# Kernel tuning notes

Hardware: AMD Instinct MI355X
Metric: run time of the kernel (lower is better)

## Reference

```python
import jax, jax.numpy as jnp
import numpy as np

T, B, X, F, Z, H = 64, 512, 784, 64, 64, 512


def _lin(v, W, b):
    return v @ W.T + b


def _gru(xt, h, Wih, Whh, bih, bhh):
    # PyTorch GRUCell gate math
    gi = xt @ Wih.T + bih
    gh = h @ Whh.T + bhh
    ir, iz, in_ = jnp.split(gi, 3, axis=-1)
    hr, hz, hn = jnp.split(gh, 3, axis=-1)
    r = jax.nn.sigmoid(ir + hr)
    z = jax.nn.sigmoid(iz + hz)
    n = jnp.tanh(in_ + r * hn)
    return (1.0 - z) * n + z * h


def _kld(mu1, sd1, mu2, sd2):
    r = sd1 / sd2
    return 0.5 * jnp.sum(((mu1 - mu2) / sd2) ** 2 + r ** 2 - 2.0 * jnp.log(r) - 1.0)


def setup_inputs() -> dict:
    key = jax.random.key(0)
    ks = iter(jax.random.split(key, 64))

    def Wn(*shape):
        return 0.02 * jax.random.normal(next(ks), shape, jnp.float32)

    d = {}
    d["x"] = jax.random.uniform(next(ks), (T, B, X), jnp.float32)
    d["eps_f"] = jax.random.normal(next(ks), (B, F), jnp.float32)
    d["eps_z"] = jax.random.normal(next(ks), (T, B, Z), jnp.float32)
    d.update(
        pxW1=Wn(H, X), pxb1=Wn(H), pxW2=Wn(H, H), pxb2=Wn(H),
        pzW=Wn(H, Z), pzb=Wn(H),
        pfW=Wn(H, F), pfb=Wn(H),
        rWih=Wn(3 * H, 3 * H), rWhh=Wn(3 * H, H), rbih=Wn(3 * H), rbhh=Wn(3 * H),
        zpW=Wn(H, H), zpb=Wn(H), zpmW=Wn(Z, H), zpmb=Wn(Z), zpsW=Wn(Z, H), zpsb=Wn(Z),
        feWih=Wn(3 * H, H), feWhh=Wn(3 * H, H), febih=Wn(3 * H), febhh=Wn(3 * H),
        femW=Wn(F, H), femb=Wn(F), fesW=Wn(F, H), fesb=Wn(F),
        zeW1=Wn(H, 2 * H), zeb1=Wn(H), zeW2=Wn(H, H), zeb2=Wn(H),
        zemW=Wn(Z, H), zemb=Wn(Z), zesW=Wn(Z, H), zesb=Wn(Z),
        dW1=Wn(H, 3 * H), db1=Wn(H), dW2=Wn(H, H), db2=Wn(H),
        dmW=Wn(X, H), dmb=Wn(X),
    )
    return d


def reference(x, eps_f, eps_z, pxW1, pxb1, pxW2, pxb2, pzW, pzb, pfW, pfb,
              rWih, rWhh, rbih, rbhh, zpW, zpb, zpmW, zpmb, zpsW, zpsb,
              feWih, feWhh, febih, febhh, femW, femb, fesW, fesb,
              zeW1, zeb1, zeW2, zeb2, zemW, zemb, zesW, zesb,
              dW1, db1, dW2, db2, dmW, dmb):
    relu = jax.nn.relu
    # phi_x over all timesteps at once: [T, B, H]
    phi_x = relu(_lin(relu(_lin(x, pxW1, pxb1)), pxW2, pxb2))
    h0 = jnp.zeros((x.shape[1], H), x.dtype)

    # f encoder GRU over the sequence; only the final hidden is used
    f_h, _ = jax.lax.scan(
        lambda h, xt: (_gru(xt, h, feWih, feWhh, febih, febhh), None), h0, phi_x)
    f_mean = _lin(f_h, femW, femb)
    f_std = jax.nn.softplus(_lin(f_h, fesW, fesb))
    f = eps_f * f_std + f_mean
    phi_f = relu(_lin(f, pfW, pfb))
    f_kld = _kld(f_mean, f_std, jnp.zeros_like(f_mean), jnp.ones_like(f_std))

    def step(carry, inp):
        h, zk, nll = carry
        px_t, e_t, x_t = inp
        zp = relu(_lin(h, zpW, zpb))
        zpm = _lin(zp, zpmW, zpmb)
        zps = jax.nn.softplus(_lin(zp, zpsW, zpsb))
        ze = relu(_lin(relu(_lin(jnp.concatenate([px_t, h], 1), zeW1, zeb1)), zeW2, zeb2))
        zem = _lin(ze, zemW, zemb)
        zes = jax.nn.softplus(_lin(ze, zesW, zesb))
        z_t = e_t * zes + zem
        phi_z = relu(_lin(z_t, pzW, pzb))
        dec = relu(_lin(relu(_lin(jnp.concatenate([phi_z, phi_f, h], 1), dW1, db1)), dW2, db2))
        dec_mean = jax.nn.sigmoid(_lin(dec, dmW, dmb))
        h_new = _gru(jnp.concatenate([px_t, phi_z, phi_f], 1), h, rWih, rWhh, rbih, rbhh)
        zk = zk + _kld(zem, zes, zpm, zps)
        nll = nll - jnp.sum(x_t * jnp.log(dec_mean) + (1.0 - x_t) * jnp.log(1.0 - dec_mean))
        return (h_new, zk, nll), None

    zero = jnp.zeros((), x.dtype)
    (_, z_kld, nll), _ = jax.lax.scan(step, (h0, zero, zero), (phi_x, eps_z, x))
    return (f_kld, z_kld, nll)
```

## Files before the change

kernel.cpp:

```cpp
#include <hip/hip_runtime.h>
#include <cmath>

namespace {

constexpr int Tn = 64;
constexpr int Bn = 512;
constexpr int Xn = 784;
constexpr int XnP = 800;
constexpr int Fn = 64;
constexpr int Zn = 64;
constexpr int Hn = 512;

typedef unsigned short us;
typedef __attribute__((ext_vector_type(8))) short bf16x8;
typedef __attribute__((ext_vector_type(4))) float f32x4;

__device__ __forceinline__ us f2b(float v) {
  unsigned int u = __float_as_uint(v);
  return (us)((u + 0x7FFFu + ((u >> 16) & 1u)) >> 16);
}
__device__ __forceinline__ float b2f(us u) { return __uint_as_float(((unsigned int)u) << 16); }
__device__ __forceinline__ float sigmf(float v) { return 1.0f / (1.0f + __expf(-v)); }
__device__ __forceinline__ float splusf(float v) {
  return v > 0.0f ? (v + log1pf(__expf(-v))) : log1pf(__expf(v));
}
__device__ __forceinline__ float block_sum(float v, float* red) {
  #pragma unroll
  for (int off = 32; off > 0; off >>= 1) v += __shfl_down(v, off, 64);
  if ((threadIdx.x & 63) == 0) red[threadIdx.x >> 6] = v;
  __syncthreads();
  float s = 0.0f;
  if (threadIdx.x == 0) s = red[0] + red[1] + red[2] + red[3];
  return s;
}

__global__ void cvt(const float* __restrict__ s, us* __restrict__ d, int n) {
  int i = blockIdx.x * 256 + threadIdx.x;
  if (i < n) d[i] = f2b(s[i]);
}
__global__ void cvt_pad(const float* __restrict__ s, us* __restrict__ d, int C, int Cp, int n) {
  int i = blockIdx.x * 256 + threadIdx.x;
  if (i < n) {
    int r = i / Cp, c = i - r * Cp;
    d[i] = (c < C) ? f2b(s[(size_t)r * C + c]) : (us)0;
  }
}

template <int NSEG, bool RELU, bool F32OUT, bool HASINIT, bool HASBIAS>
__device__ void tile_gemmx(
    int bx, int by,
    const us* A0, const us* W0, int ldw0, int K0,
    const us* A1, const us* W1, int ldw1, int K1,
    const float* initC, int ldi, const float* bias,
    void* Cout, int ldc, char* smemc)
{
  us* As = (us*)smemc; us* Bs = (us*)(smemc + 5120);
  const int tid = threadIdx.x, srow = tid >> 2, scb = (tid & 3) * 8;
  const int lane = tid & 63, w = tid >> 6, l15 = lane & 15, q = lane >> 4;
  const int m0 = by * 64, n0 = bx * 64;
  f32x4 acc[4];
  if (HASINIT) {
    #pragma unroll
    for (int j = 0; j < 4; ++j)
      #pragma unroll
      for (int r = 0; r < 4; ++r)
        acc[j][r] = initC[(size_t)(m0 + w * 16 + q * 4 + r) * ldi + n0 + j * 16 + l15];
  } else {
    #pragma unroll
    for (int j = 0; j < 4; ++j) acc[j] = (f32x4){0.f, 0.f, 0.f, 0.f};
  }
  #pragma unroll
  for (int seg = 0; seg < NSEG; ++seg) {
    const us* A = (seg == 0) ? A0 : A1;
    const us* W = (seg == 0) ? W0 : W1;
    const int ldw = (seg == 0) ? ldw0 : ldw1;
    const int K   = (seg == 0) ? K0 : K1;
    const us* ap = A + (size_t)(m0 + srow) * K + scb;
    const us* wp = W + (size_t)(n0 + srow) * ldw + scb;
    uint4 av = *(const uint4*)ap;
    uint4 wv = *(const uint4*)wp;
    for (int k0 = 0; k0 < K; k0 += 32) {
      __syncthreads();
      *(uint4*)&As[srow * 40 + scb] = av;
      *(uint4*)&Bs[srow * 40 + scb] = wv;
      __syncthreads();
      if (k0 + 32 < K) {
        av = *(const uint4*)(ap + k0 + 32);
        wv = *(const uint4*)(wp + k0 + 32);
      }
      bf16x8 a = *(const bf16x8*)&As[(w * 16 + l15) * 40 + q * 8];
      #pragma unroll
      for (int j = 0; j < 4; ++j) {
        bf16x8 b = *(const bf16x8*)&Bs[(j * 16 + l15) * 40 + q * 8];
        acc[j] = __builtin_amdgcn_mfma_f32_16x16x32_bf16(a, b, acc[j], 0, 0, 0);
      }
    }
  }
  #pragma unroll
  for (int j = 0; j < 4; ++j) {
    const int col = n0 + j * 16 + l15;
    const float bv = HASBIAS ? bias[col] : 0.f;
    #pragma unroll
    for (int r = 0; r < 4; ++r) {
      const int row = m0 + w * 16 + q * 4 + r;
      float v = acc[j][r] + bv;
      if (RELU) v = fmaxf(v, 0.f);
      if (F32OUT) ((float*)Cout)[(size_t)row * ldc + col] = v;
      else        ((us*)Cout)[(size_t)row * ldc + col] = f2b(v);
    }
  }
}

__device__ void tile_gru_fe(
    int bx, int by,
    const us* A0, const us* Wih,
    const us* hprev, const us* Whh,
    const float* bih, const float* bhh,
    us* hnew, char* smemc)
{
  us* Asm = (us*)smemc; us* Rs = (us*)(smemc + 5120);
  us* Zs = (us*)(smemc + 10240); us* Ns = (us*)(smemc + 15360);
  const int tid = threadIdx.x, srow = tid >> 2, scb = (tid & 3) * 8;
  const int lane = tid & 63, w = tid >> 6, l15 = lane & 15, q = lane >> 4;
  const int m0 = by * 64, c0 = bx * 64;
  f32x4 aR[4], aZ[4], aI[4], aH[4];
  #pragma unroll
  for (int j = 0; j < 4; ++j) {
    aR[j] = (f32x4){0.f, 0.f, 0.f, 0.f}; aZ[j] = aR[j]; aI[j] = aR[j]; aH[j] = aR[j];
  }
  #pragma unroll
  for (int seg = 0; seg < 2; ++seg) {
    const bool hseg = (seg == 1);
    const us* A  = hseg ? hprev : A0;
    const us* Wb = hseg ? Whh : Wih;
    const us* ap = A + (size_t)(m0 + srow) * Hn + scb;
    const us* wr = Wb + (size_t)(c0 + srow) * Hn + scb;
    const us* wz = wr + (size_t)Hn * Hn;
    const us* wn = wz + (size_t)Hn * Hn;
    uint4 av = *(const uint4*)ap;
    uint4 rv = *(const uint4*)wr;
    uint4 zv = *(const uint4*)wz;
// ... 24 lines not shown
      }
    }
  }
  #pragma unroll
  for (int j = 0; j < 4; ++j) {
    const int c = c0 + j * 16 + l15;
    const float bR = bih[c] + bhh[c];
    const float bZ = bih[Hn + c] + bhh[Hn + c];
    const float bI = bih[2 * Hn + c];
    const float bH = bhh[2 * Hn + c];
    #pragma unroll
    for (int r = 0; r < 4; ++r) {
      const int m = m0 + w * 16 + q * 4 + r;
      const float h = b2f(hprev[(size_t)m * Hn + c]);
      const float rg = sigmf(aR[j][r] + bR);
      const float zg = sigmf(aZ[j][r] + bZ);
      const float ng = tanhf(aI[j][r] + bI + rg * (aH[j][r] + bH));
      hnew[(size_t)m * Hn + c] = f2b((1.0f - zg) * ng + zg * h);
    }
  }
}

__device__ void tile_gru_fin(
    int bx, int by,
    const us* phiz, const us* rWih,
    const float* gipre, const float* ghpre,
    const us* hprev,
    const float* bih, const float* bhh,
    us* hnew, char* smemc)
{
  us* Asm = (us*)smemc; us* Rs = (us*)(smemc + 5120);
  us* Zs = (us*)(smemc + 10240); us* Ns = (us*)(smemc + 15360);
  const int tid = threadIdx.x, srow = tid >> 2, scb = (tid & 3) * 8;
  const int lane = tid & 63, w = tid >> 6, l15 = lane & 15, q = lane >> 4;
  const int m0 = by * 64, c0 = bx * 64;
  f32x4 aR[4], aZ[4], aI[4];
  float aH[4][4];
  #pragma unroll
  for (int j = 0; j < 4; ++j) {
    const int c = c0 + j * 16 + l15;
    #pragma unroll
    for (int r = 0; r < 4; ++r) {
      const size_t row = (size_t)(m0 + w * 16 + q * 4 + r) * 1536;
      aR[j][r] = gipre[row + c] + ghpre[row + c];
      aZ[j][r] = gipre[row + 512 + c] + ghpre[row + 512 + c];
      aI[j][r] = gipre[row + 1024 + c];
      aH[j][r] = ghpre[row + 1024 + c];
    }
  }
  const us* ap = phiz + (size_t)(m0 + srow) * Hn + scb;
  const us* wr = rWih + (size_t)(c0 + srow) * 1536 + 512 + scb;
  const us* wz = wr + (size_t)512 * 1536;
// ... 26 lines not shown
      aI[j] = __builtin_amdgcn_mfma_f32_16x16x32_bf16(a, bn, aI[j], 0, 0, 0);
    }
  }
  #pragma unroll
  for (int j = 0; j < 4; ++j) {
    const int c = c0 + j * 16 + l15;
    const float bR = bih[c] + bhh[c];
    const float bZ = bih[Hn + c] + bhh[Hn + c];
    const float bI = bih[2 * Hn + c];
    const float bH = bhh[2 * Hn + c];
    #pragma unroll
    for (int r = 0; r < 4; ++r) {
      const int m = m0 + w * 16 + q * 4 + r;
      const float h = b2f(hprev[(size_t)m * Hn + c]);
      const float rg = sigmf(aR[j][r] + bR);
      const float zg = sigmf(aZ[j][r] + bZ);
      const float ng = tanhf(aI[j][r] + bI + rg * (aH[j][r] + bH));
      hnew[(size_t)m * Hn + c] = f2b((1.0f - zg) * ng + zg * h);
    }
  }
}

__device__ void tile_nll(
    int bx, int by,
    const us* dec, const us* dmW, const float* dmb, const float* xt,
    float* nll, char* smemc)
{
  us* As = (us*)smemc; us* Bs = (us*)(smemc + 5120);
  float* red = (float*)(smemc + 10240);
  const int tid = threadIdx.x, srow = tid >> 2, scb = (tid & 3) * 8;
  const int lane = tid & 63, w = tid >> 6, l15 = lane & 15, q = lane >> 4;
  const int m0 = by * 64, n0 = bx * 64;
  f32x4 acc[4];
  #pragma unroll
  for (int j = 0; j < 4; ++j) acc[j] = (f32x4){0.f, 0.f, 0.f, 0.f};
  const int wrow = (n0 + srow < Xn) ? (n0 + srow) : (Xn - 1);
  const us* ap = dec + (size_t)(m0 + srow) * Hn + scb;
  const us* wp = dmW + (size_t)wrow * Hn + scb;
  uint4 av = *(const uint4*)ap;
  uint4 wv = *(const uint4*)wp;
  for (int k0 = 0; k0 < Hn; k0 += 32) {
    __syncthreads();
    *(uint4*)&As[srow * 40 + scb] = av;
    *(uint4*)&Bs[srow * 40 + scb] = wv;
    __syncthreads();
    if (k0 + 32 < Hn) {
      av = *(const uint4*)(ap + k0 + 32);
      wv = *(const uint4*)(wp + k0 + 32);
    }
// ... 6 lines not shown
  }
  float sum = 0.0f;
  #pragma unroll
  for (int j = 0; j < 4; ++j) {
    const int n = n0 + j * 16 + l15;
    if (n < Xn) {
      const float bv = dmb[n];
      #pragma unroll
      for (int r = 0; r < 4; ++r) {
        const int m = m0 + w * 16 + q * 4 + r;
        const float a = acc[j][r] + bv;
        const float xv = xt[(size_t)m * Xn + n];
        sum += splusf(-a) + (1.0f - xv) * a;
      }
    }
  }
  const float s = block_sum(sum, red);
  if (tid == 0) atomicAdd(nll, s);
}

template <int MODE>
__device__ void stat_dual(int vb,
    const us* Ain, const us* Wm, const float* bm, const us* Ws, const float* bs,
    const float* eps, const float* pm_in, const float* ps_in,
    us* o0b, float* o_pm, float* o_ps, float* kacc, char* smemc)
{
  us* As = (us*)smemc; us* Ms = (us*)(smemc + 5120); us* Ss = (us*)(smemc + 10240);
  float* red = (float*)(smemc + 15360);
  const int tid = threadIdx.x, srow = tid >> 2, scb = (tid & 3) * 8;
  const int lane = tid & 63, w = tid >> 6, l15 = lane & 15, q = lane >> 4;
  const int m0 = vb * 64;
  f32x4 am[4], as_[4];
  #pragma unroll
  for (int j = 0; j < 4; ++j) { am[j] = (f32x4){0.f, 0.f, 0.f, 0.f}; as_[j] = am[j]; }
  const us* ap = Ain + (size_t)(m0 + srow) * Hn + scb;
  const us* mp = Wm + (size_t)srow * Hn + scb;
  const us* sp = Ws + (size_t)srow * Hn + scb;
  uint4 av = *(const uint4*)ap;
  uint4 mv = *(const uint4*)mp;
  uint4 sv = *(const uint4*)sp;
  for (int k0 = 0; k0 < Hn; k0 += 32) {
    __syncthreads();
    *(uint4*)&As[srow * 40 + scb] = av;
    *(uint4*)&Ms[srow * 40 + scb] = mv;
    *(uint4*)&Ss[srow * 40 + scb] = sv;
    __syncthreads();
    if (k0 + 32 < Hn) {
      av = *(const uint4*)(ap + k0 + 32);
// ... 4 lines not shown
    #pragma unroll
    for (int j = 0; j < 4; ++j) {
      bf16x8 b0 = *(const bf16x8*)&Ms[(j * 16 + l15) * 40 + q * 8];
      bf16x8 b1 = *(const bf16x8*)&Ss[(j * 16 + l15) * 40 + q * 8];
      am[j]  = __builtin_amdgcn_mfma_f32_16x16x32_bf16(a, b0, am[j], 0, 0, 0);
      as_[j] = __builtin_amdgcn_mfma_f32_16x16x32_bf16(a, b1, as_[j], 0, 0, 0);
    }
  }
  float kld = 0.0f;
  #pragma unroll
  for (int j = 0; j < 4; ++j) {
    const int c = j * 16 + l15;
    const float bmv = bm[c], bsv = bs[c];
    #pragma unroll
    for (int r = 0; r < 4; ++r) {
      const int m = m0 + w * 16 + q * 4 + r;
      const float mu = am[j][r] + bmv;
      const float sd = splusf(as_[j][r] + bsv);
      if (MODE == 0) {
        o_pm[(size_t)m * Zn + c] = mu;
        o_ps[(size_t)m * Zn + c] = sd;
      } else {
        o0b[(size_t)m * Zn + c] = f2b(eps[(size_t)m * Zn + c] * sd + mu);
        if (MODE == 1) {
          kld += mu * mu + sd * sd - 2.0f * __logf(sd) - 1.0f;
        } else {
          const float pm = pm_in[(size_t)m * Zn + c];
          const float ps = ps_in[(size_t)m * Zn + c];
          const float dd = (mu - pm) / ps;
          const float rr = sd / ps;
          kld += dd * dd + rr * rr - 2.0f * __logf(rr) - 1.0f;
        }
      }
    }
  }
  if (MODE != 0) {
    const float s = block_sum(kld, red);
    if (tid == 0) atomicAdd(kacc, 0.5f * s);
  }
}

__global__ __launch_bounds__(256) void k_gemmA(
    const us* A, const us* W, int ldw, int K, const float* bias, us* C, int ldc)
{
  __shared__ alignas(16) char sm[10240];
  tile_gemmx<1, true, false, false, true>(blockIdx.x, blockIdx.y, A, W, ldw, K,
      nullptr, nullptr, 0, 0, nullptr, 0, bias, C, ldc, sm);
}

__global__ __launch_bounds__(256) void k_gruB(
    const us* A0, const us* Wih, const us* hprev, const us* Whh,
    const float* bih, const float* bhh, us* hnew)
{
  __shared__ alignas(16) char sm[20480];
  tile_gru_fe(blockIdx.x, blockIdx.y, A0, Wih, hprev, Whh, bih, bhh, hnew, sm);
}

__global__ __launch_bounds__(256) void k_statf(
    const us* fh, const us* femW, const float* femb, const us* fesW, const float* fesb,
    const float* eps_f, us* fbuf, float* kacc)
{
  __shared__ alignas(16) char sm[15376];
  stat_dual<1>(blockIdx.x, fh, femW, femb, fesW, fesb, eps_f,
               nullptr, nullptr, fbuf, nullptr, nullptr, kacc, sm);
}

__global__ __launch_bounds__(256) void kP2(
    const us* phi_f, const us* rWih, const us* dW1, const float* db1,
    float* Cpre_gru, float* Cpre_dec)
{
  __shared__ alignas(16) char sm[10240];
  const int b = blockIdx.x;
  if (b < 192)
    tile_gemmx<1, false, true, false, false>(b % 24, b / 24, phi_f, rWih + 1024, 1536, Hn,
        nullptr, nullptr, 0, 0, nullptr, 0, nullptr, Cpre_gru, 1536, sm);
  else
    tile_gemmx<1, false, true, false, true>((b - 192) & 7, (b - 192) >> 3,
        phi_f, dW1 + 512, 1536, Hn,
        nullptr, nullptr, 0, 0, nullptr, 0, db1, Cpre_dec, 512, sm);
}

__global__ __launch_bounds__(256) void kP3(
    const us* h0, const us* zpW, const float* zpb, us* zp,
    const us* px0, const us* zeW1, const float* zeb1, us* zepre)
{
  __shared__ alignas(16) char sm[10240];
  const int b = blockIdx.x;
  if (b < 64)
    tile_gemmx<1, true, false, false, true>(b & 7, b >> 3, h0, zpW, Hn, Hn,
        nullptr, nullptr, 0, 0, nullptr, 0, zpb, zp, Hn, sm);
  else
    tile_gemmx<2, true, false, false, true>((b - 64) & 7, (b - 64) >> 3,
        px0, zeW1, 1024, Hn, h0, zeW1 + 512, 1024, Hn,
        nullptr, 0, zeb1, zepre, Hn, sm);
}

__global__ __launch_bounds__(256) void kP4(
    const us* zepre, const us* zeW2, const float* zeb2, us* ze,
    const us* zp, const us* zpmW, const float* zpmb, const us* zpsW, const float* zpsb,
    float* zpm, float* zps)
{
  __shared__ alignas(16) char sm[15376];
  const int b = blockIdx.x;
  if (b < 64)
    tile_gemmx<1, true, false, false, true>(b & 7, b >> 3, zepre, zeW2, Hn, Hn,
        nullptr, nullptr, 0, 0, nullptr, 0, zeb2, ze, Hn, sm);
  else
    stat_dual<0>(b - 64, zp, zpmW, zpmb, zpsW, zpsb,
                 nullptr, nullptr, nullptr, nullptr, zpm, zps, nullptr, sm);
}

__global__ __launch_bounds__(256) void kS1(
    const us* ze, const us* zemW, const float* zemb, const us* zesW, const float* zesb,
    const float* eps_zt, const float* zpm, const float* zps, us* zt, float* kacc,
    const us* px_t, const us* rWih, const float* Cpre_gru, float* gipre)
{
  __shared__ alignas(16) char sm[15376];
  const int b = blockIdx.x;
  if (b < 8)
    stat_dual<2>(b, ze, zemW, zemb, zesW, zesb, eps_zt, zpm, zps,
                 zt, nullptr, nullptr, kacc, sm);
  else {
    const int tb = b - 8;
    tile_gemmx<1, false, true, true, false>(tb % 24, tb / 24, px_t, rWih, 1536, Hn,
        nullptr, nullptr, 0, 0, Cpre_gru, 1536, nullptr, gipre, 1536, sm);
  }
}

__global__ __launch_bounds__(256) void kS2(
    const us* zt, const us* pzW, const float* pzb, us* phiz)
{
  __shared__ alignas(16) char sm[10240];
  tile_gemmx<1, true, false, false, true>(blockIdx.x & 7, blockIdx.x >> 3, zt, pzW, Zn, Zn,
      nullptr, nullptr, 0, 0, nullptr, 0, pzb, phiz, Hn, sm);
}

__global__ __launch_bounds__(256) void kS3(
    const us* phiz, const us* rWih, const float* gipre, const float* ghpre,
    const us* hprev, const float* rbih, const float* rbhh, us* hnew,
    const us* dW1, const float* dtmph, us* dtmp)
{
  __shared__ alignas(16) char sm[20480];
  const int b = blockIdx.x;
  if (b < 64)
    tile_gru_fin(b & 7, b >> 3, phiz, rWih, gipre, ghpre, hprev, rbih, rbhh, hnew, sm);
  else
    tile_gemmx<1, true, false, true, false>((b - 64) & 7, (b - 64) >> 3, phiz, dW1, 1536, Hn,
        nullptr, nullptr, 0, 0, dtmph, 512, nullptr, dtmp, Hn, sm);
}

__global__ __launch_bounds__(256) void kS4(
    const us* dtmp, const us* dW2, const float* db2, us* dec,
    const us* hnext, const us* zpW, const float* zpb, us* zp,
    const us* px1, const us* zeW1, const float* zeb1, us* zepre,
    const us* dW1, const float* Cpre_dec, float* dtmph)
{
  __shared__ alignas(16) char sm[10240];
  const int b = blockIdx.x;
  if (b < 64)
    tile_gemmx<1, true, false, false, true>(b & 7, b >> 3, dtmp, dW2, Hn, Hn,
        nullptr, nullptr, 0, 0, nullptr, 0, db2, dec, Hn, sm);
  else if (b < 128)
    tile_gemmx<1, true, false, false, true>((b - 64) & 7, (b - 64) >> 3, hnext, zpW, Hn, Hn,
        nullptr, nullptr, 0, 0, nullptr, 0, zpb, zp, Hn, sm);
  else if (b < 192)
    tile_gemmx<2, true, false, false, true>((b - 128) & 7, (b - 128) >> 3,
        px1, zeW1, 1024, Hn, hnext, zeW1 + 512, 1024, Hn,
        nullptr, 0, zeb1, zepre, Hn, sm);
  else
    tile_gemmx<1, false, true, true, false>((b - 192) & 7, (b - 192) >> 3,
        hnext, dW1 + 1024, 1536, Hn,
        nullptr, nullptr, 0, 0, Cpre_dec, 512, nullptr, dtmph, 512, sm);
}

__global__ __launch_bounds__(256) void kS5(
    const us* dec, const us* dmW, const float* dmb, const float* xt, float* nll,
    const us* zepre, const us* zeW2, const float* zeb2, us* ze,
    const us* zp, const us* zpmW, const float* zpmb, const us* zpsW, const float* zpsb,
    float* zpm, float* zps,
    const us* hnext, const us* rWhh, float* ghpre)
{
  __shared__ alignas(16) char sm[15376];
  const int b = blockIdx.x;
  if (b < 104)
    tile_nll(b % 13, b / 13, dec, dmW, dmb, xt, nll, sm);
  else if (b < 168)
    tile_gemmx<1, true, false, false, true>((b - 104) & 7, (b - 104) >> 3, zepre, zeW2, Hn, Hn,
        nullptr, nullptr, 0, 0, nullptr, 0, zeb2, ze, Hn, sm);
  else if (b < 176)
    stat_dual<0>(b - 168, zp, zpmW, zpmb, zpsW, zpsb,
                 nullptr, nullptr, nullptr, nullptr, zpm, zps, nullptr, sm);
  else {
    const int tb = b - 176;
    tile_gemmx<1, false, true, false, false>(tb % 24, tb / 24, hnext, rWhh, Hn, Hn,
        nullptr, nullptr, 0, 0, nullptr, 0, nullptr, ghpre, 1536, sm);
  }
}

}

extern "C" void kernel_launch(void* const* d_in, const int* in_sizes, int n_in,
                              void* d_out, int out_size, void* d_ws, size_t ws_size,
                              hipStream_t stream)
{
  (void)in_sizes; (void)n_in; (void)out_size;
  const float* x     = (const float*)d_in[0];
  const float* eps_f = (const float*)d_in[1];
  const float* eps_z = (const float*)d_in[2];
  const float* pxW1  = (const float*)d_in[3];
  const float* pxb1  = (const float*)d_in[4];
  const float* pxW2  = (const float*)d_in[5];
  const float* pxb2  = (const float*)d_in[6];
  const float* pzW   = (const float*)d_in[7];
  const float* pzb   = (const float*)d_in[8];
  const float* pfW   = (const float*)d_in[9];
  const float* pfb   = (const float*)d_in[10];
  const float* rWih  = (const float*)d_in[11];
  const float* rWhh  = (const float*)d_in[12];
  const float* rbih  = (const float*)d_in[13];
  const float* rbhh  = (const float*)d_in[14];
  const float* zpW   = (const float*)d_in[15];
  const float* zpb   = (const float*)d_in[16];
  const float* zpmW  = (const float*)d_in[17];
  const float* zpmb  = (const float*)d_in[18];
  const float* zpsW  = (const float*)d_in[19];
  const float* zpsb  = (const float*)d_in[20];
  const float* feWih = (const float*)d_in[21];
  const float* feWhh = (const float*)d_in[22];
// ... 28 lines not shown
  };

  us* b_pxW1  = (us*)ab((size_t)512 * XnP * 2);
  us* b_pxW2  = (us*)ab((size_t)512 * 512 * 2);
  us* b_pzW   = (us*)ab((size_t)512 * 64 * 2);
  us* b_pfW   = (us*)ab((size_t)512 * 64 * 2);
  us* b_rWih  = (us*)ab((size_t)1536 * 1536 * 2);
  us* b_rWhh  = (us*)ab((size_t)1536 * 512 * 2);
  us* b_zpW   = (us*)ab((size_t)512 * 512 * 2);
  us* b_zpmW  = (us*)ab((size_t)64 * 512 * 2);
  us* b_zpsW  = (us*)ab((size_t)64 * 512 * 2);
  us* b_feWih = (us*)ab((size_t)1536 * 512 * 2);
  us* b_feWhh = (us*)ab((size_t)1536 * 512 * 2);
  us* b_femW  = (us*)ab((size_t)64 * 512 * 2);
  us* b_fesW  = (us*)ab((size_t)64 * 512 * 2);
  us* b_zeW1  = (us*)ab((size_t)512 * 1024 * 2);
  us* b_zeW2  = (us*)ab((size_t)512 * 512 * 2);
  us* b_zemW  = (us*)ab((size_t)64 * 512 * 2);
  us* b_zesW  = (us*)ab((size_t)64 * 512 * 2);
  us* b_dW1   = (us*)ab((size_t)512 * 1536 * 2);
  us* b_dW2   = (us*)ab((size_t)512 * 512 * 2);
  us* b_dmW   = (us*)ab((size_t)Xn * 512 * 2);

  us* phi_x = (us*)ab((size_t)Tn * Bn * Hn * 2);
  us* fh_a  = (us*)ab((size_t)Bn * Hn * 2);
  us* h_a   = (us*)ab((size_t)Bn * Hn * 2);
  us* fh_b  = (us*)ab((size_t)Bn * Hn * 2);
  us* h_b   = (us*)ab((size_t)Bn * Hn * 2);
  us* fbuf  = (us*)ab((size_t)Bn * Fn * 2);
  us* phi_f = (us*)ab((size_t)Bn * Hn * 2);
  us* zp    = (us*)ab((size_t)Bn * Hn * 2);
  us* zepre = (us*)ab((size_t)Bn * Hn * 2);
  us* ze    = (us*)ab((size_t)Bn * Hn * 2);
  us* zt    = (us*)ab((size_t)Bn * Zn * 2);
  us* phiz  = (us*)ab((size_t)Bn * Hn * 2);
  us* dtmp  = (us*)ab((size_t)Bn * Hn * 2);
  us* dec   = (us*)ab((size_t)Bn * Hn * 2);
  float* zpm = (float*)ab((size_t)Bn * Zn * 4);
  float* zps = (float*)ab((size_t)Bn * Zn * 4);
  float* Cpre_gru = (float*)ab((size_t)Bn * 1536 * 4);
  float* Cpre_dec = (float*)ab((size_t)Bn * 512 * 4);
  float* gipre    = (float*)ab((size_t)Bn * 1536 * 4);
  float* ghpre    = (float*)ab((size_t)Bn * 1536 * 4);
  float* dtmph    = (float*)ab((size_t)Bn * 512 * 4);

  int CH = 16;
  while (CH > 1 && off + (size_t)CH * (Bn * XnP + Bn * Hn) * 2 + 4096 > ws_size) CH >>= 1;
  us* xch  = (us*)ab((size_t)CH * Bn * XnP * 2);
  us* tmpb = (us*)ab((size_t)CH * Bn * Hn * 2);

  hipMemsetAsync(d_out, 0, 3 * sizeof(float), stream);
  hipMemsetAsync(fh_a, 0, 2 * (size_t)Bn * Hn * 2, stream);
  hipMemsetAsync(ghpre, 0, (size_t)Bn * 1536 * 4, stream);

  const dim3 blk(256);
  auto CVT = [&](const float* s, us* d, size_t n) {
    cvt<<<dim3((unsigned)((n + 255) / 256)), blk, 0, stream>>>(s, d, (int)n);
  };

  {
    const size_t n = (size_t)512 * XnP;
    cvt_pad<<<dim3((unsigned)((n + 255) / 256)), blk, 0, stream>>>(pxW1, b_pxW1, Xn, XnP, (int)n);
  }
  CVT(pxW2, b_pxW2, (size_t)512 * 512);
  CVT(pzW, b_pzW, (size_t)512 * 64);
  CVT(pfW, b_pfW, (size_t)512 * 64);
  CVT(rWih, b_rWih, (size_t)1536 * 1536);
  CVT(rWhh, b_rWhh, (size_t)1536 * 512);
  CVT(zpW, b_zpW, (size_t)512 * 512);
  CVT(zpmW, b_zpmW, (size_t)64 * 512);
  CVT(zpsW, b_zpsW, (size_t)64 * 512);
  CVT(feWih, b_feWih, (size_t)1536 * 512);
  CVT(feWhh, b_feWhh, (size_t)1536 * 512);
  CVT(femW, b_femW, (size_t)64 * 512);
  CVT(fesW, b_fesW, (size_t)64 * 512);
  CVT(zeW1, b_zeW1, (size_t)512 * 1024);
  CVT(zeW2, b_zeW2, (size_t)512 * 512);
  CVT(zemW, b_zemW, (size_t)64 * 512);
  CVT(zesW, b_zesW, (size_t)64 * 512);
  CVT(dW1, b_dW1, (size_t)512 * 1536);
  CVT(dW2, b_dW2, (size_t)512 * 512);
  CVT(dmW, b_dmW, (size_t)Xn * 512);

  for (int c = 0; c < Tn / CH; ++c) {
    const size_t nx = (size_t)CH * Bn * XnP;
    cvt_pad<<<dim3((unsigned)((nx + 255) / 256)), blk, 0, stream>>>(
        x + (size_t)c * CH * Bn * Xn, xch, Xn, XnP, (int)nx);
    const dim3 gA(8, CH * Bn / 64);
    k_gemmA<<<gA, blk, 0, stream>>>(xch, b_pxW1, XnP, XnP, pxb1, tmpb, Hn);
    k_gemmA<<<gA, blk, 0, stream>>>(tmpb, b_pxW2, Hn, Hn, pxb2,
                                    phi_x + (size_t)c * CH * Bn * Hn, Hn);
  }

  us* fc = fh_a; us* fn2 = fh_b;
  for (int t = 0; t < Tn; ++t) {
    k_gruB<<<dim3(8, 8), blk, 0, stream>>>(
        phi_x + (size_t)t * Bn * Hn, b_feWih, fc, b_feWhh, febih, febhh, fn2);
    us* sw = fc; fc = fn2; fn2 = sw;
  }

  k_statf<<<dim3(8), blk, 0, stream>>>(fh_a, b_femW, femb, b_fesW, fesb, eps_f, fbuf, out + 0);

  k_gemmA<<<dim3(8, 8), blk, 0, stream>>>(fbuf, b_pfW, Fn, Fn, pfb, phi_f, Hn);
  kP2<<<dim3(256), blk, 0, stream>>>(phi_f, b_rWih, b_dW1, db1, Cpre_gru, Cpre_dec);
  hipMemcpyAsync(dtmph, Cpre_dec, (size_t)Bn * 512 * 4, hipMemcpyDeviceToDevice, stream);
  kP3<<<dim3(128), blk, 0, stream>>>(h_a, b_zpW, zpb, zp, phi_x, b_zeW1, zeb1, zepre);
  kP4<<<dim3(72), blk, 0, stream>>>(zepre, b_zeW2, zeb2, ze,
                                    zp, b_zpmW, zpmb, b_zpsW, zpsb, zpm, zps);

  for (int t = 0; t < Tn; ++t) {
    const us* hcur = (t & 1) ? h_b : h_a;
    us* hnext      = (t & 1) ? h_a : h_b;
    const bool last = (t == Tn - 1);
    const us* px_t = phi_x + (size_t)t * Bn * Hn;

    kS1<<<dim3(200), blk, 0, stream>>>(
        ze, b_zemW, zemb, b_zesW, zesb, eps_z + (size_t)t * Bn * Zn, zpm, zps,
        zt, out + 1, px_t, b_rWih, Cpre_gru, gipre);

    kS2<<<dim3(64), blk, 0, stream>>>(zt, b_pzW, pzb, phiz);

    kS3<<<dim3(128), blk, 0, stream>>>(
        phiz, b_rWih, gipre, ghpre, hcur, rbih, rbhh, hnext,
        b_dW1, dtmph, dtmp);

    kS4<<<dim3(last ? 64 : 256), blk, 0, stream>>>(
        dtmp, b_dW2, db2, dec,
        hnext, b_zpW, zpb, zp,
        phi_x + (size_t)(t + 1) * Bn * Hn, b_zeW1, zeb1, zepre,
        b_dW1, Cpre_dec, dtmph);

    kS5<<<dim3(last ? 104 : 368), blk, 0, stream>>>(
        dec, b_dmW, dmb, x + (size_t)t * Bn * Xn, out + 2,
        zepre, b_zeW2, zeb2, ze,
        zp, b_zpmW, zpmb, b_zpsW, zpsb, zpm, zps,
        hnext, b_rWhh, ghpre);
  }
}
```

Measured before the change: 6.581 ms.

## Fuse x conversion into first GEMM, precompute phi_x zeW1 part, merge per-step kernels

Replaces the chunked x-to-bf16 conversion plus GEMM with one GEMM that converts fp32 x on load. It precomputes the phi_x half of the ze encoder's first layer for all timesteps in bulk, so each step only multiplies h. The z stat/KLD kernel now also computes phi_z in the same block, removing one launch per step. The prologue kernels are merged and the dtmph memcpy is dropped by pointer selection. This costs extra workspace for two full [T,B,H] buffers and puts heavier work in the 8 statphiz blocks.

```diff
diff --git a/kernel.cpp b/kernel.cpp
--- a/kernel.cpp
+++ b/kernel.cpp
@@ -46,12 +46,12 @@
   }
 }
 
-template <int NSEG, bool RELU, bool F32OUT, bool HASINIT, bool HASBIAS>
+template <int NSEG, bool RELU, bool F32OUT, int IMODE, bool HASBIAS>
 __device__ void tile_gemmx(
     int bx, int by,
     const us* A0, const us* W0, int ldw0, int K0,
     const us* A1, const us* W1, int ldw1, int K1,
-    const float* initC, int ldi, const float* bias,
+    const float* initF, const us* initB, int ldi, const float* bias,
     void* Cout, int ldc, char* smemc)
 {
   us* As = (us*)smemc; us* Bs = (us*)(smemc + 5120);
@@ -59,12 +59,12 @@
   const int lane = tid & 63, w = tid >> 6, l15 = lane & 15, q = lane >> 4;
   const int m0 = by * 64, n0 = bx * 64;
   f32x4 acc[4];
-  if (HASINIT) {
+  if (IMODE == 1) {
     #pragma unroll
     for (int j = 0; j < 4; ++j)
       #pragma unroll
       for (int r = 0; r < 4; ++r)
-        acc[j][r] = initC[(size_t)(m0 + w * 16 + q * 4 + r) * ldi + n0 + j * 16 + l15];
+        acc[j][r] = initF[(size_t)(m0 + w * 16 + q * 4 + r) * ldi + n0 + j * 16 + l15];
   } else {
     #pragma unroll
     for (int j = 0; j < 4; ++j) acc[j] = (f32x4){0.f, 0.f, 0.f, 0.f};
@@ -104,6 +104,7 @@
     for (int r = 0; r < 4; ++r) {
       const int row = m0 + w * 16 + q * 4 + r;
       float v = acc[j][r] + bv;
+      if (IMODE == 2) v += b2f(initB[(size_t)row * ldi + col]);
       if (RELU) v = fmaxf(v, 0.f);
       if (F32OUT) ((float*)Cout)[(size_t)row * ldc + col] = v;
       else        ((us*)Cout)[(size_t)row * ldc + col] = f2b(v);
@@ -111,12 +112,63 @@
   }
 }
 
+__device__ void tile_gA1(int bx, int by, const float* __restrict__ X, const us* W,
+                         const float* bias, us* C, char* smemc)
+{
+  us* As = (us*)smemc; us* Bs = (us*)(smemc + 5120);
+  const int tid = threadIdx.x, srow = tid >> 2, scb = (tid & 3) * 8;
+  const int lane = tid & 63, w = tid >> 6, l15 = lane & 15, q = lane >> 4;
+  const int m0 = by * 64, n0 = bx * 64;
+  f32x4 acc[4];
+  #pragma unroll
+  for (int j = 0; j < 4; ++j) acc[j] = (f32x4){0.f, 0.f, 0.f, 0.f};
+  auto ldA = [&](int k) -> uint4 {
+    if (k + scb < Xn) {
+      const float* p = X + (size_t)(m0 + srow) * Xn + k + scb;
+      float4 f0 = *(const float4*)p;
+      float4 f1 = *(const float4*)(p + 4);
+      union { us h[8]; uint4 u; } pk;
+      pk.h[0] = f2b(f0.x); pk.h[1] = f2b(f0.y); pk.h[2] = f2b(f0.z); pk.h[3] = f2b(f0.w);
+      pk.h[4] = f2b(f1.x); pk.h[5] = f2b(f1.y); pk.h[6] = f2b(f1.z); pk.h[7] = f2b(f1.w);
+      return pk.u;
+    }
+    return (uint4){0, 0, 0, 0};
+  };
+  const us* wp = W + (size_t)(n0 + srow) * XnP + scb;
+  uint4 av = ldA(0);
+  uint4 wv = *(const uint4*)wp;
+  for (int k0 = 0; k0 < XnP; k0 += 32) {
+    __syncthreads();
+    *(uint4*)&As[srow * 40 + scb] = av;
+    *(uint4*)&Bs[srow * 40 + scb] = wv;
+    __syncthreads();
+    if (k0 + 32 < XnP) {
+      av = ldA(k0 + 32);
+      wv = *(const uint4*)(wp + k0 + 32);
+    }
+    bf16x8 a = *(const bf16x8*)&As[(w * 16 + l15) * 40 + q * 8];
+    #pragma unroll
+    for (int j = 0; j < 4; ++j) {
+      bf16x8 b = *(const bf16x8*)&Bs[(j * 16 + l15) * 40 + q * 8];
+      acc[j] = __builtin_amdgcn_mfma_f32_16x16x32_bf16(a, b, acc[j], 0, 0, 0);
+    }
+  }
+  #pragma unroll
+  for (int j = 0; j < 4; ++j) {
+    const int col = n0 + j * 16 + l15;
+    const float bv = bias[col];
+    #pragma unroll
+    for (int r = 0; r < 4; ++r) {
+      const int row = m0 + w * 16 + q * 4 + r;
+      C[(size_t)row * Hn + col] = f2b(fmaxf(acc[j][r] + bv, 0.f));
+    }
+  }
+}
+
 __device__ void tile_gru_fe(
-    int bx, int by,
-    const us* A0, const us* Wih,
+    int bx, int by, const us* A0, const us* Wih,
     const us* hprev, const us* Whh,
-    const float* bih, const float* bhh,
-    us* hnew, char* smemc)
+    const float* bih, const float* bhh, us* hnew, char* smemc)
 {
   us* Asm = (us*)smemc; us* Rs = (us*)(smemc + 5120);
   us* Zs = (us*)(smemc + 10240); us* Ns = (us*)(smemc + 15360);
@@ -187,12 +239,9 @@
 }
 
 __device__ void tile_gru_fin(
-    int bx, int by,
-    const us* phiz, const us* rWih,
-    const float* gipre, const float* ghpre,
-    const us* hprev,
-    const float* bih, const float* bhh,
-    us* hnew, char* smemc)
+    int bx, int by, const us* phiz, const us* rWih,
+    const float* gipre, const float* ghpre, const us* hprev,
+    const float* bih, const float* bhh, us* hnew, char* smemc)
 {
   us* Asm = (us*)smemc; us* Rs = (us*)(smemc + 5120);
   us* Zs = (us*)(smemc + 10240); us* Ns = (us*)(smemc + 15360);
@@ -265,9 +314,8 @@
 }
 
 __device__ void tile_nll(
-    int bx, int by,
-    const us* dec, const us* dmW, const float* dmb, const float* xt,
-    float* nll, char* smemc)
+    int bx, int by, const us* dec, const us* dmW, const float* dmb,
+    const float* xt, float* nll, char* smemc)
 {
   us* As = (us*)smemc; us* Bs = (us*)(smemc + 5120);
   float* red = (float*)(smemc + 10240);
@@ -320,8 +368,7 @@
 template <int MODE>
 __device__ void stat_dual(int vb,
     const us* Ain, const us* Wm, const float* bm, const us* Ws, const float* bs,
-    const float* eps, const float* pm_in, const float* ps_in,
-    us* o0b, float* o_pm, float* o_ps, float* kacc, char* smemc)
+    const float* eps, us* o0b, float* o_pm, float* o_ps, float* kacc, char* smemc)
 {
   us* As = (us*)smemc; us* Ms = (us*)(smemc + 5120); us* Ss = (us*)(smemc + 10240);
   float* red = (float*)(smemc + 15360);
@@ -372,15 +419,7 @@
         o_ps[(size_t)m * Zn + c] = sd;
       } else {
         o0b[(size_t)m * Zn + c] = f2b(eps[(size_t)m * Zn + c] * sd + mu);
-        if (MODE == 1) {
-          kld += mu * mu + sd * sd - 2.0f * __logf(sd) - 1.0f;
-        } else {
-          const float pm = pm_in[(size_t)m * Zn + c];
-          const float ps = ps_in[(size_t)m * Zn + c];
-          const float dd = (mu - pm) / ps;
-          const float rr = sd / ps;
-          kld += dd * dd + rr * rr - 2.0f * __logf(rr) - 1.0f;
-        }
+        kld += mu * mu + sd * sd - 2.0f * __logf(sd) - 1.0f;
       }
     }
   }
@@ -390,15 +429,121 @@
   }
 }
 
-__global__ __launch_bounds__(256) void k_gemmA(
+__device__ void statphiz(int vb,
+    const us* ze, const us* Wm, const float* bm, const us* Ws, const float* bs,
+    const float* eps, const float* zpm, const float* zps,
+    const us* pzW, const float* pzb, us* phiz, float* kacc, char* smemc)
+{
+  us* As = (us*)smemc; us* Ms = (us*)(smemc + 5120); us* Ss = (us*)(smemc + 10240);
+  us* ztL = (us*)(smemc + 15360);
+  float* red = (float*)(smemc + 24576);
+  const int tid = threadIdx.x, srow = tid >> 2, scb = (tid & 3) * 8;
+  const int lane = tid & 63, w = tid >> 6, l15 = lane & 15, q = lane >> 4;
+  const int m0 = vb * 64;
+  f32x4 am[4], as_[4];
+  #pragma unroll
+  for (int j = 0; j < 4; ++j) { am[j] = (f32x4){0.f, 0.f, 0.f, 0.f}; as_[j] = am[j]; }
+  const us* ap = ze + (size_t)(m0 + srow) * Hn + scb;
+  const us* mp = Wm + (size_t)srow * Hn + scb;
+  const us* sp = Ws + (size_t)srow * Hn + scb;
+  uint4 av = *(const uint4*)ap;
+  uint4 mv = *(const uint4*)mp;
+  uint4 sv = *(const uint4*)sp;
+  for (int k0 = 0; k0 < Hn; k0 += 32) {
+    __syncthreads();
+    *(uint4*)&As[srow * 40 + scb] = av;
+    *(uint4*)&Ms[srow * 40 + scb] = mv;
+    *(uint4*)&Ss[srow * 40 + scb] = sv;
+    __syncthreads();
+    if (k0 + 32 < Hn) {
+      av = *(const uint4*)(ap + k0 + 32);
+      mv = *(const uint4*)(mp + k0 + 32);
+      sv = *(const uint4*)(sp + k0 + 32);
+    }
+    bf16x8 a = *(const bf16x8*)&As[(w * 16 + l15) * 40 + q * 8];
+    #pragma unroll
+    for (int j = 0; j < 4; ++j) {
+      bf16x8 b0 = *(const bf16x8*)&Ms[(j * 16 + l15) * 40 + q * 8];
+      bf16x8 b1 = *(const bf16x8*)&Ss[(j * 16 + l15) * 40 + q * 8];
+      am[j]  = __builtin_amdgcn_mfma_f32_16x16x32_bf16(a, b0, am[j], 0, 0, 0);
+      as_[j] = __builtin_amdgcn_mfma_f32_16x16x32_bf16(a, b1, as_[j], 0, 0, 0);
+    }
+  }
+  float kld = 0.0f;
+  #pragma unroll
+  for (int j = 0; j < 4; ++j) {
+    const int c = j * 16 + l15;
+    const float bmv = bm[c], bsv = bs[c];
+    #pragma unroll
+    for (int r = 0; r < 4; ++r) {
+      const int row = w * 16 + q * 4 + r;
+      const int m = m0 + row;
+      const float mu = am[j][r] + bmv;
+      const float sd = splusf(as_[j][r] + bsv);
+      ztL[row * 72 + c] = f2b(eps[(size_t)m * Zn + c] * sd + mu);
+      const float pm = zpm[(size_t)m * Zn + c];
+      const float ps = zps[(size_t)m * Zn + c];
+      const float dd = (mu - pm) / ps;
+      const float rr = sd / ps;
+      kld += dd * dd + rr * rr - 2.0f * __logf(rr) - 1.0f;
+    }
+  }
+  const float s = block_sum(kld, red);
+  if (tid == 0) atomicAdd(kacc, 0.5f * s);
+  for (int cc = 0; cc < 8; ++cc) {
+    f32x4 acc[4];
+    #pragma unroll
+    for (int j = 0; j < 4; ++j) acc[j] = (f32x4){0.f, 0.f, 0.f, 0.f};
+    #pragma unroll
+    for (int k0 = 0; k0 < 64; k0 += 32) {
+      uint4 wv = *(const uint4*)(pzW + (size_t)(cc * 64 + srow) * 64 + k0 + scb);
+      __syncthreads();
+      *(uint4*)&As[srow * 40 + scb] = wv;
+      __syncthreads();
+      bf16x8 a = *(const bf16x8*)&ztL[(w * 16 + l15) * 72 + k0 + q * 8];
+      #pragma unroll
+      for (int j = 0; j < 4; ++j) {
+        bf16x8 b = *(const bf16x8*)&As[(j * 16 + l15) * 40 + q * 8];
+        acc[j] = __builtin_amdgcn_mfma_f32_16x16x32_bf16(a, b, acc[j], 0, 0, 0);
+      }
+    }
+    #pragma unroll
+    for (int j = 0; j < 4; ++j) {
+      const int col = cc * 64 + j * 16 + l15;
+      const float bz = pzb[col];
+      #pragma unroll
+      for (int r = 0; r < 4; ++r) {
+        const int row = w * 16 + q * 4 + r;
+        phiz[(size_t)(m0 + row) * Hn + col] = f2b(fmaxf(acc[j][r] + bz, 0.f));
+      }
+    }
+  }
+}
+
+__global__ __launch_bounds__(256) void g_A1(
+    const float* X, const us* W, const float* bias, us* C)
+{
+  __shared__ alignas(16) char sm[10240];
+  tile_gA1(blockIdx.x, blockIdx.y, X, W, bias, C, sm);
+}
+
+__global__ __launch_bounds__(256) void g_gemm(
     const us* A, const us* W, int ldw, int K, const float* bias, us* C, int ldc)
 {
   __shared__ alignas(16) char sm[10240];
-  tile_gemmx<1, true, false, false, true>(blockIdx.x, blockIdx.y, A, W, ldw, K,
-      nullptr, nullptr, 0, 0, nullptr, 0, bias, C, ldc, sm);
-}
-
-__global__ __launch_bounds__(256) void k_gruB(
+  tile_gemmx<1, true, false, 0, true>(blockIdx.x, blockIdx.y, A, W, ldw, K,
+      nullptr, nullptr, 0, 0, nullptr, nullptr, 0, bias, C, ldc, sm);
+}
+
+__global__ __launch_bounds__(256) void g_bulkZE(
+    const us* A, const us* zeW1, us* out)
+{
+  __shared__ alignas(16) char sm[10240];
+  tile_gemmx<1, false, false, 0, false>(blockIdx.x, blockIdx.y, A, zeW1, 1024, Hn,
+      nullptr, nullptr, 0, 0, nullptr, nullptr, 0, nullptr, out, Hn, sm);
+}
+
+__global__ __launch_bounds__(256) void g_gruB(
     const us* A0, const us* Wih, const us* hprev, const us* Whh,
     const float* bih, const float* bhh, us* hnew)
 {
@@ -406,46 +551,40 @@
   tile_gru_fe(blockIdx.x, blockIdx.y, A0, Wih, hprev, Whh, bih, bhh, hnew, sm);
 }
 
-__global__ __launch_bounds__(256) void k_statf(
+__global__ __launch_bounds__(256) void g_statf(
     const us* fh, const us* femW, const float* femb, const us* fesW, const float* fesb,
     const float* eps_f, us* fbuf, float* kacc)
 {
   __shared__ alignas(16) char sm[15376];
   stat_dual<1>(blockIdx.x, fh, femW, femb, fesW, fesb, eps_f,
-               nullptr, nullptr, fbuf, nullptr, nullptr, kacc, sm);
-}
-
-__global__ __launch_bounds__(256) void kP2(
+               fbuf, nullptr, nullptr, kacc, sm);
+}
+
+__global__ __launch_bounds__(256) void g_P23(
     const us* phi_f, const us* rWih, const us* dW1, const float* db1,
-    float* Cpre_gru, float* Cpre_dec)
+    float* Cpre_gru, float* Cpre_dec,
+    const us* h0, const us* zpW, const float* zpb, us* zp,
+    const us* zeprePX0, const us* zeW1, const float* zeb1, us* zepre)
 {
   __shared__ alignas(16) char sm[10240];
   const int b = blockIdx.x;
   if (b < 192)
-    tile_gemmx<1, false, true, false, false>(b % 24, b / 24, phi_f, rWih + 1024, 1536, Hn,
-        nullptr, nullptr, 0, 0, nullptr, 0, nullptr, Cpre_gru, 1536, sm);
+    tile_gemmx<1, false, true, 0, false>(b % 24, b / 24, phi_f, rWih + 1024, 1536, Hn,
+        nullptr, nullptr, 0, 0, nullptr, nullptr, 0, nullptr, Cpre_gru, 1536, sm);
+  else if (b < 256)
+    tile_gemmx<1, false, true, 0, true>((b - 192) & 7, (b - 192) >> 3,
+        phi_f, dW1 + 512, 1536, Hn, nullptr, nullptr, 0, 0,
+        nullptr, nullptr, 0, db1, Cpre_dec, 512, sm);
+  else if (b < 320)
+    tile_gemmx<1, true, false, 0, true>((b - 256) & 7, (b - 256) >> 3, h0, zpW, Hn, Hn,
+        nullptr, nullptr, 0, 0, nullptr, nullptr, 0, zpb, zp, Hn, sm);
   else
-    tile_gemmx<1, false, true, false, true>((b - 192) & 7, (b - 192) >> 3,
-        phi_f, dW1 + 512, 1536, Hn,
-        nullptr, nullptr, 0, 0, nullptr, 0, db1, Cpre_dec, 512, sm);
-}
-
-__global__ __launch_bounds__(256) void kP3(
-    const us* h0, const us* zpW, const float* zpb, us* zp,
-    const us* px0, const us* zeW1, const float* zeb1, us* zepre)
-{
-  __shared__ alignas(16) char sm[10240];
-  const int b = blockIdx.x;
-  if (b < 64)
-    tile_gemmx<1, true, false, false, true>(b & 7, b >> 3, h0, zpW, Hn, Hn,
-        nullptr, nullptr, 0, 0, nullptr, 0, zpb, zp, Hn, sm);
-  else
-    tile_gemmx<2, true, false, false, true>((b - 64) & 7, (b - 64) >> 3,
-        px0, zeW1, 1024, Hn, h0, zeW1 + 512, 1024, Hn,
-        nullptr, 0, zeb1, zepre, Hn, sm);
-}
-
-__global__ __launch_bounds__(256) void kP4(
+    tile_gemmx<1, true, false, 2, true>((b - 320) & 7, (b - 320) >> 3,
+        h0, zeW1 + 512, 1024, Hn, nullptr, nullptr, 0, 0,
+        nullptr, zeprePX0, 512, zeb1, zepre, Hn, sm);
+}
+
+__global__ __launch_bounds__(256) void g_P4(
     const us* zepre, const us* zeW2, const float* zeb2, us* ze,
     const us* zp, const us* zpmW, const float* zpmb, const us* zpsW, const float* zpsb,
     float* zpm, float* zps)
@@ -453,39 +592,32 @@
   __shared__ alignas(16) char sm[15376];
   const int b = blockIdx.x;
   if (b < 64)
-    tile_gemmx<1, true, false, false, true>(b & 7, b >> 3, zepre, zeW2, Hn, Hn,
-        nullptr, nullptr, 0, 0, nullptr, 0, zeb2, ze, Hn, sm);
+    tile_gemmx<1, true, false, 0, true>(b & 7, b >> 3, zepre, zeW2, Hn, Hn,
+        nullptr, nullptr, 0, 0, nullptr, nullptr, 0, zeb2, ze, Hn, sm);
   else
     stat_dual<0>(b - 64, zp, zpmW, zpmb, zpsW, zpsb,
-                 nullptr, nullptr, nullptr, nullptr, zpm, zps, nullptr, sm);
-}
-
-__global__ __launch_bounds__(256) void kS1(
+                 nullptr, nullptr, zpm, zps, nullptr, sm);
+}
+
+__global__ __launch_bounds__(256) void g_A(
     const us* ze, const us* zemW, const float* zemb, const us* zesW, const float* zesb,
-    const float* eps_zt, const float* zpm, const float* zps, us* zt, float* kacc,
+    const float* eps_zt, const float* zpm, const float* zps,
+    const us* pzW, const float* pzb, us* phiz, float* kacc,
     const us* px_t, const us* rWih, const float* Cpre_gru, float* gipre)
 {
-  __shared__ alignas(16) char sm[15376];
+  __shared__ alignas(16) char sm[24832];
   const int b = blockIdx.x;
   if (b < 8)
-    stat_dual<2>(b, ze, zemW, zemb, zesW, zesb, eps_zt, zpm, zps,
-                 zt, nullptr, nullptr, kacc, sm);
+    statphiz(b, ze, zemW, zemb, zesW, zesb, eps_zt, zpm, zps,
+             pzW, pzb, phiz, kacc, sm);
   else {
     const int tb = b - 8;
-    tile_gemmx<1, false, true, true, false>(tb % 24, tb / 24, px_t, rWih, 1536, Hn,
-        nullptr, nullptr, 0, 0, Cpre_gru, 1536, nullptr, gipre, 1536, sm);
-  }
-}
-
-__global__ __launch_bounds__(256) void kS2(
-    const us* zt, const us* pzW, const float* pzb, us* phiz)
-{
-  __shared__ alignas(16) char sm[10240];
-  tile_gemmx<1, true, false, false, true>(blockIdx.x & 7, blockIdx.x >> 3, zt, pzW, Zn, Zn,
-      nullptr, nullptr, 0, 0, nullptr, 0, pzb, phiz, Hn, sm);
-}
-
-__global__ __launch_bounds__(256) void kS3(
+    tile_gemmx<1, false, true, 1, false>(tb % 24, tb / 24, px_t, rWih, 1536, Hn,
+        nullptr, nullptr, 0, 0, Cpre_gru, nullptr, 1536, nullptr, gipre, 1536, sm);
+  }
+}
+
+__global__ __launch_bounds__(256) void g_B(
     const us* phiz, const us* rWih, const float* gipre, const float* ghpre,
     const us* hprev, const float* rbih, const float* rbhh, us* hnew,
     const us* dW1, const float* dtmph, us* dtmp)
@@ -495,35 +627,35 @@
   if (b < 64)
     tile_gru_fin(b & 7, b >> 3, phiz, rWih, gipre, ghpre, hprev, rbih, rbhh, hnew, sm);
   else
-    tile_gemmx<1, true, false, true, false>((b - 64) & 7, (b - 64) >> 3, phiz, dW1, 1536, Hn,
-        nullptr, nullptr, 0, 0, dtmph, 512, nullptr, dtmp, Hn, sm);
-}
-
-__global__ __launch_bounds__(256) void kS4(
+    tile_gemmx<1, true, false, 1, false>((b - 64) & 7, (b - 64) >> 3, phiz, dW1, 1536, Hn,
+        nullptr, nullptr, 0, 0, dtmph, nullptr, 512, nullptr, dtmp, Hn, sm);
+}
+
+__global__ __launch_bounds__(256) void g_C(
     const us* dtmp, const us* dW2, const float* db2, us* dec,
     const us* hnext, const us* zpW, const float* zpb, us* zp,
-    const us* px1, const us* zeW1, const float* zeb1, us* zepre,
+    const us* zeprePX1, const us* zeW1, const float* zeb1, us* zepre,
     const us* dW1, const float* Cpre_dec, float* dtmph)
 {
   __shared__ alignas(16) char sm[10240];
   const int b = blockIdx.x;
   if (b < 64)
-    tile_gemmx<1, true, false, false, true>(b & 7, b >> 3, dtmp, dW2, Hn, Hn,
-        nullptr, nullptr, 0, 0, nullptr, 0, db2, dec, Hn, sm);
+    tile_gemmx<1, true, false, 0, true>(b & 7, b >> 3, dtmp, dW2, Hn, Hn,
+        nullptr, nullptr, 0, 0, nullptr, nullptr, 0, db2, dec, Hn, sm);
   else if (b < 128)
-    tile_gemmx<1, true, false, false, true>((b - 64) & 7, (b - 64) >> 3, hnext, zpW, Hn, Hn,
-        nullptr, nullptr, 0, 0, nullptr, 0, zpb, zp, Hn, sm);
+    tile_gemmx<1, true, false, 0, true>((b - 64) & 7, (b - 64) >> 3, hnext, zpW, Hn, Hn,
+        nullptr, nullptr, 0, 0, nullptr, nullptr, 0, zpb, zp, Hn, sm);
   else if (b < 192)
-    tile_gemmx<2, true, false, false, true>((b - 128) & 7, (b - 128) >> 3,
-        px1, zeW1, 1024, Hn, hnext, zeW1 + 512, 1024, Hn,
-        nullptr, 0, zeb1, zepre, Hn, sm);
+    tile_gemmx<1, true, false, 2, true>((b - 128) & 7, (b - 128) >> 3,
+        hnext, zeW1 + 512, 1024, Hn, nullptr, nullptr, 0, 0,
+        nullptr, zeprePX1, 512, zeb1, zepre, Hn, sm);
   else
-    tile_gemmx<1, false, true, true, false>((b - 192) & 7, (b - 192) >> 3,
-        hnext, dW1 + 1024, 1536, Hn,
-        nullptr, nullptr, 0, 0, Cpre_dec, 512, nullptr, dtmph, 512, sm);
-}
-
-__global__ __launch_bounds__(256) void kS5(
+    tile_gemmx<1, false, true, 1, false>((b - 192) & 7, (b - 192) >> 3,
+        hnext, dW1 + 1024, 1536, Hn, nullptr, nullptr, 0, 0,
+        Cpre_dec, nullptr, 512, nullptr, dtmph, 512, sm);
+}
+
+__global__ __launch_bounds__(256) void g_D(
     const us* dec, const us* dmW, const float* dmb, const float* xt, float* nll,
     const us* zepre, const us* zeW2, const float* zeb2, us* ze,
     const us* zp, const us* zpmW, const float* zpmb, const us* zpsW, const float* zpsb,
@@ -535,15 +667,15 @@
   if (b < 104)
     tile_nll(b % 13, b / 13, dec, dmW, dmb, xt, nll, sm);
   else if (b < 168)
-    tile_gemmx<1, true, false, false, true>((b - 104) & 7, (b - 104) >> 3, zepre, zeW2, Hn, Hn,
-        nullptr, nullptr, 0, 0, nullptr, 0, zeb2, ze, Hn, sm);
+    tile_gemmx<1, true, false, 0, true>((b - 104) & 7, (b - 104) >> 3, zepre, zeW2, Hn, Hn,
+        nullptr, nullptr, 0, 0, nullptr, nullptr, 0, zeb2, ze, Hn, sm);
   else if (b < 176)
     stat_dual<0>(b - 168, zp, zpmW, zpmb, zpsW, zpsb,
-                 nullptr, nullptr, nullptr, nullptr, zpm, zps, nullptr, sm);
+                 nullptr, nullptr, zpm, zps, nullptr, sm);
   else {
     const int tb = b - 176;
-    tile_gemmx<1, false, true, false, false>(tb % 24, tb / 24, hnext, rWhh, Hn, Hn,
-        nullptr, nullptr, 0, 0, nullptr, 0, nullptr, ghpre, 1536, sm);
+    tile_gemmx<1, false, true, 0, false>(tb % 24, tb / 24, hnext, rWhh, Hn, Hn,
+        nullptr, nullptr, 0, 0, nullptr, nullptr, 0, nullptr, ghpre, 1536, sm);
   }
 }
 
@@ -553,7 +685,7 @@
                               void* d_out, int out_size, void* d_ws, size_t ws_size,
                               hipStream_t stream)
 {
-  (void)in_sizes; (void)n_in; (void)out_size;
+  (void)in_sizes; (void)n_in; (void)out_size; (void)ws_size;
   const float* x     = (const float*)d_in[0];
   const float* eps_f = (const float*)d_in[1];
   const float* eps_z = (const float*)d_in[2];
@@ -628,7 +760,9 @@
   us* b_dW2   = (us*)ab((size_t)512 * 512 * 2);
   us* b_dmW   = (us*)ab((size_t)Xn * 512 * 2);
 
-  us* phi_x = (us*)ab((size_t)Tn * Bn * Hn * 2);
+  us* phi_x   = (us*)ab((size_t)Tn * Bn * Hn * 2);
+  us* tmpA    = (us*)ab((size_t)Tn * Bn * Hn * 2);
+  us* zeprePX = (us*)ab((size_t)Tn * Bn * Hn * 2);
   us* fh_a  = (us*)ab((size_t)Bn * Hn * 2);
   us* h_a   = (us*)ab((size_t)Bn * Hn * 2);
   us* fh_b  = (us*)ab((size_t)Bn * Hn * 2);
@@ -638,7 +772,6 @@
   us* zp    = (us*)ab((size_t)Bn * Hn * 2);
   us* zepre = (us*)ab((size_t)Bn * Hn * 2);
   us* ze    = (us*)ab((size_t)Bn * Hn * 2);
-  us* zt    = (us*)ab((size_t)Bn * Zn * 2);
   us* phiz  = (us*)ab((size_t)Bn * Hn * 2);
   us* dtmp  = (us*)ab((size_t)Bn * Hn * 2);
   us* dec   = (us*)ab((size_t)Bn * Hn * 2);
@@ -649,11 +782,6 @@
   float* gipre    = (float*)ab((size_t)Bn * 1536 * 4);
   float* ghpre    = (float*)ab((size_t)Bn * 1536 * 4);
   float* dtmph    = (float*)ab((size_t)Bn * 512 * 4);
-
-  int CH = 16;
-  while (CH > 1 && off + (size_t)CH * (Bn * XnP + Bn * Hn) * 2 + 4096 > ws_size) CH >>= 1;
-  us* xch  = (us*)ab((size_t)CH * Bn * XnP * 2);
-  us* tmpb = (us*)ab((size_t)CH * Bn * Hn * 2);
 
   hipMemsetAsync(d_out, 0, 3 * sizeof(float), stream);
   hipMemsetAsync(fh_a, 0, 2 * (size_t)Bn * Hn * 2, stream);
@@ -688,55 +816,46 @@
   CVT(dW2, b_dW2, (size_t)512 * 512);
   CVT(dmW, b_dmW, (size_t)Xn * 512);
 
-  for (int c = 0; c < Tn / CH; ++c) {
-    const size_t nx = (size_t)CH * Bn * XnP;
-    cvt_pad<<<dim3((unsigned)((nx + 255) / 256)), blk, 0, stream>>>(
-        x + (size_t)c * CH * Bn * Xn, xch, Xn, XnP, (int)nx);
-    const dim3 gA(8, CH * Bn / 64);
-    k_gemmA<<<gA, blk, 0, stream>>>(xch, b_pxW1, XnP, XnP, pxb1, tmpb, Hn);
-    k_gemmA<<<gA, blk, 0, stream>>>(tmpb, b_pxW2, Hn, Hn, pxb2,
-                                    phi_x + (size_t)c * CH * Bn * Hn, Hn);
-  }
+  g_A1<<<dim3(8, Tn * Bn / 64), blk, 0, stream>>>(x, b_pxW1, pxb1, tmpA);
+  g_gemm<<<dim3(8, Tn * Bn / 64), blk, 0, stream>>>(tmpA, b_pxW2, Hn, Hn, pxb2, phi_x, Hn);
+  g_bulkZE<<<dim3(8, Tn * Bn / 64), blk, 0, stream>>>(phi_x, b_zeW1, zeprePX);
 
   us* fc = fh_a; us* fn2 = fh_b;
   for (int t = 0; t < Tn; ++t) {
-    k_gruB<<<dim3(8, 8), blk, 0, stream>>>(
+    g_gruB<<<dim3(8, 8), blk, 0, stream>>>(
         phi_x + (size_t)t * Bn * Hn, b_feWih, fc, b_feWhh, febih, febhh, fn2);
     us* sw = fc; fc = fn2; fn2 = sw;
   }
 
-  k_statf<<<dim3(8), blk, 0, stream>>>(fh_a, b_femW, femb, b_fesW, fesb, eps_f, fbuf, out + 0);
-
-  k_gemmA<<<dim3(8, 8), blk, 0, stream>>>(fbuf, b_pfW, Fn, Fn, pfb, phi_f, Hn);
-  kP2<<<dim3(256), blk, 0, stream>>>(phi_f, b_rWih, b_dW1, db1, Cpre_gru, Cpre_dec);
-  hipMemcpyAsync(dtmph, Cpre_dec, (size_t)Bn * 512 * 4, hipMemcpyDeviceToDevice, stream);
-  kP3<<<dim3(128), blk, 0, stream>>>(h_a, b_zpW, zpb, zp, phi_x, b_zeW1, zeb1, zepre);
-  kP4<<<dim3(72), blk, 0, stream>>>(zepre, b_zeW2, zeb2, ze,
-                                    zp, b_zpmW, zpmb, b_zpsW, zpsb, zpm, zps);
+  g_statf<<<dim3(8), blk, 0, stream>>>(fh_a, b_femW, femb, b_fesW, fesb, eps_f, fbuf, out + 0);
+
+  g_gemm<<<dim3(8, 8), blk, 0, stream>>>(fbuf, b_pfW, Fn, Fn, pfb, phi_f, Hn);
+  g_P23<<<dim3(384), blk, 0, stream>>>(phi_f, b_rWih, b_dW1, db1, Cpre_gru, Cpre_dec,
+                                       h_a, b_zpW, zpb, zp, zeprePX, b_zeW1, zeb1, zepre);
+  g_P4<<<dim3(72), blk, 0, stream>>>(zepre, b_zeW2, zeb2, ze,
+                                     zp, b_zpmW, zpmb, b_zpsW, zpsb, zpm, zps);
 
   for (int t = 0; t < Tn; ++t) {
     const us* hcur = (t & 1) ? h_b : h_a;
     us* hnext      = (t & 1) ? h_a : h_b;
     const bool last = (t == Tn - 1);
     const us* px_t = phi_x + (size_t)t * Bn * Hn;
-
-    kS1<<<dim3(200), blk, 0, stream>>>(
+    const float* dtmph_sel = (t == 0) ? Cpre_dec : dtmph;
+
+    g_A<<<dim3(200), blk, 0, stream>>>(
         ze, b_zemW, zemb, b_zesW, zesb, eps_z + (size_t)t * Bn * Zn, zpm, zps,
-        zt, out + 1, px_t, b_rWih, Cpre_gru, gipre);
-
-    kS2<<<dim3(64), blk, 0, stream>>>(zt, b_pzW, pzb, phiz);
-
-    kS3<<<dim3(128), blk, 0, stream>>>(
+        b_pzW, pzb, phiz, out + 1, px_t, b_rWih, Cpre_gru, gipre);
+
+    g_B<<<dim3(128), blk, 0, stream>>>(
         phiz, b_rWih, gipre, ghpre, hcur, rbih, rbhh, hnext,
-        b_dW1, dtmph, dtmp);
-
-    kS4<<<dim3(last ? 64 : 256), blk, 0, stream>>>(
-        dtmp, b_dW2, db2, dec,
-        hnext, b_zpW, zpb, zp,
-        phi_x + (size_t)(t + 1) * Bn * Hn, b_zeW1, zeb1, zepre,
+        b_dW1, dtmph_sel, dtmp);
+
+    g_C<<<dim3(last ? 64 : 256), blk, 0, stream>>>(
+        dtmp, b_dW2, db2, dec, hnext, b_zpW, zpb, zp,
+        zeprePX + (size_t)(t + 1) * Bn * Hn, b_zeW1, zeb1, zepre,
         b_dW1, Cpre_dec, dtmph);
 
-    kS5<<<dim3(last ? 104 : 368), blk, 0, stream>>>(
+    g_D<<<dim3(last ? 104 : 368), blk, 0, stream>>>(
         dec, b_dmW, dmb, x + (size_t)t * Bn * Xn, out + 2,
         zepre, b_zeW2, zeb2, ze,
         zp, b_zpmW, zpmb, b_zpsW, zpsb, zpm, zps,
```

Result: slower. 6.854 ms (+4.1%).
